# Kernel tuning notes

Hardware: AMD Instinct MI355X
Metric: run time of the kernel (lower is better)

The kernel has to match this reference:

```python
import jax, jax.numpy as jnp
import numpy as np
from jax import lax

B, N, S, H = 8, 32, 512, 768   # batch, max spans, seq len, bert hidden
K, C, L = 3, 128, 64           # conv kernel height, cnn_hidden_size, num labels


def setup_inputs() -> dict:
    key = jax.random.key(0)
    ks = jax.random.split(key, 9)
    rng = np.random.default_rng(0)
    W = 16  # max span width
    starts = rng.integers(0, S - W, size=(B, N))
    widths = rng.integers(1, W + 1, size=(B, N))
    starts[0, 0], widths[0, 0] = 100, W        # force max span width = 16
    starts[0, 1], widths[0, 1] = S - W, 1      # force max prefix width = 496
    starts[0, 2], widths[0, 2] = 0, 1          # force min end = 1 -> max suffix = 511
    ends = starts + widths
    spans_dranges = jnp.asarray(np.stack([starts, ends], axis=-1), dtype=jnp.int32)
    sc = 0.02
    return {
        "tokens_emb": jax.random.normal(ks[0], (B, S, H), jnp.float32),
        "span_w": jax.random.normal(ks[1], (C, H, K), jnp.float32) * sc,
        "span_b": jax.random.normal(ks[2], (C,), jnp.float32) * sc,
        "prefix_w": jax.random.normal(ks[3], (C, H, K), jnp.float32) * sc,
        "prefix_b": jax.random.normal(ks[4], (C,), jnp.float32) * sc,
        "suffix_w": jax.random.normal(ks[5], (C, H, K), jnp.float32) * sc,
        "suffix_b": jax.random.normal(ks[6], (C,), jnp.float32) * sc,
        "fc_w": jax.random.normal(ks[7], (L, 3 * C), jnp.float32) * sc,
        "fc_b": jax.random.normal(ks[8], (L,), jnp.float32) * sc,
        "spans_dranges": spans_dranges,
        "word_seq_lengths": jnp.full((B,), S, dtype=jnp.int32),
        "max_span_width": W,
        "max_prefix_width": S - W,
        "max_suffix_width": S - 1,
    }


def _conv_pool(x, w, b):
    # x: [BN, T, H]; Conv2d(H->C, kernel (K,1)) over time + max_pool over all valid positions
    T = x.shape[1]
    if T < K:  # original pads with zeros up to kernel size
        x = jnp.pad(x, ((0, 0), (0, K - T), (0, 0)))
    y = lax.conv_general_dilated(x.transpose(0, 2, 1), w, (1,), 'VALID',
                                 dimension_numbers=('NCH', 'OIH', 'NCH'))  # [BN, C, T-K+1]
    return (y + b[None, :, None]).max(axis=2)  # pool_filter_size == full output length


def reference(tokens_emb, span_w, span_b, prefix_w, prefix_b, suffix_w, suffix_b,
              fc_w, fc_b, spans_dranges, word_seq_lengths,
              max_span_width, max_prefix_width, max_suffix_width):
    starts = spans_dranges[..., 0]  # [B,N]
    ends = spans_dranges[..., 1]

    def gather(idx, mask):
        # idx, mask: [B,N,W] -> zero-padded per-span token embeddings [B*N, W, H]
        g = jnp.take_along_axis(tokens_emb[:, None], jnp.clip(idx, 0, S - 1)[..., None], axis=2)
        return (g * mask[..., None]).reshape(B * N, -1, H)

    ar = jnp.arange(max_span_width)
    span_x = gather(starts[..., None] + ar, ar < (ends - starts)[..., None])
    arp = jnp.arange(max_prefix_width)
    prefix_x = gather(jnp.broadcast_to(arp, (B, N, max_prefix_width)), arp < starts[..., None])
    ars = jnp.arange(max_suffix_width)
    suffix_x = gather(ends[..., None] + ars,
                      ars < (word_seq_lengths[:, None, None] - ends[..., None]))

    feats = jnp.concatenate([
        _conv_pool(prefix_x, prefix_w, prefix_b),
        _conv_pool(span_x, span_w, span_b),
        _conv_pool(suffix_x, suffix_w, suffix_b),
    ], axis=-1)  # [B*N, 3C]
    probs = jax.nn.sigmoid(feats @ fc_w.T + fc_b)  # [B*N, L]
    pred_ids = (probs > 0.5).astype(jnp.int32).reshape(B, N, L)
    return probs, pred_ids
```

## Files before the change

### kernel.cpp

```cpp
#include <hip/hip_runtime.h>
#include <hip/hip_bf16.h>
#include <math.h>

#define NEG_INF (-1e30f)

typedef _Float16 half8 __attribute__((ext_vector_type(8)));
typedef _Float16 half4 __attribute__((ext_vector_type(4)));
typedef float f32x4 __attribute__((ext_vector_type(4)));
typedef float f32x16 __attribute__((ext_vector_type(16)));

__device__ __forceinline__ void load_lds16(const void* g, void* l) {
  __builtin_amdgcn_global_load_lds((const __attribute__((address_space(1))) void*)g,
                                   (__attribute__((address_space(3))) void*)l, 16, 0, 0);
}

__global__ __launch_bounds__(256) void prep(
    const float* __restrict__ tokens, const float* __restrict__ span_w,
    const float* __restrict__ prefix_w, const float* __restrict__ suffix_w,
    const float* __restrict__ fc_w, _Float16* __restrict__ A2,
    _Float16* __restrict__ Bt, float* __restrict__ fcT) {
  int bid = blockIdx.x;
  int t = threadIdx.x;
  if (bid < 3072) {
    int g4 = (bid * 256 + t) * 4;
    int m = g4 / 768, h = g4 % 768;
    float4 x = *(const float4*)(tokens + g4);
    float xs[4] = {x.x, x.y, x.z, x.w};
    half4 hi, lo;
#pragma unroll
    for (int i = 0; i < 4; ++i) {
      _Float16 h_ = (_Float16)xs[i];
      hi[i] = h_;
      lo[i] = (_Float16)((xs[i] - (float)h_) * 64.0f);
    }
    size_t base = (size_t)m * 1536 + h;
    *(half4*)(A2 + base) = hi;
    *(half4*)(A2 + base + 768) = lo;
  } else if (bid < 3216) {
    int g = (bid - 3072) * 256 + t;
    int ws = g / 12288;
    int r = g % 12288;
    int c = r / 96, h = (r % 96) * 8;
    const float* wsrc = (ws == 0) ? prefix_w : (ws == 1) ? span_w : suffix_w;
    const float* src = wsrc + (size_t)(c * 768 + h) * 3;
    float wv[24];
#pragma unroll
    for (int i = 0; i < 6; ++i) *(float4*)&wv[i * 4] = *(const float4*)(src + i * 4);
#pragma unroll
    for (int tap = 0; tap < 3; ++tap) {
      half8 hi, lo;
#pragma unroll
      for (int i = 0; i < 8; ++i) {
        float x = wv[i * 3 + tap];
        _Float16 h_ = (_Float16)x;
        hi[i] = h_;
        lo[i] = (_Float16)((x - (float)h_) * 64.0f);
      }
      size_t jb = (size_t)(ws * 384 + tap * 128 + c) * 1536 + h;
      *(half8*)(Bt + jb) = hi;
      *(half8*)(Bt + jb + 768) = lo;
    }
  } else {
    int g = (bid - 3216) * 256 + t;
    int i = g >> 6, c = g & 63;
    fcT[g] = fc_w[c * 384 + i];
  }
}

__global__ __launch_bounds__(512) void gemm_f16(const _Float16* __restrict__ A2,
                                                const _Float16* __restrict__ Bt,
                                                float* __restrict__ Ct) {
  __shared__ _Float16 As[2][128 * 64];
  __shared__ _Float16 Bs[2][64 * 64];
  const int bm = blockIdx.x * 128;
  const int bj = blockIdx.y * 64;
  const int tid = threadIdx.x;
  const int w = tid >> 6;
  const int lane = tid & 63;
  const int lrow = lane >> 3;
  const int cphys = lane & 7;
  const int clog = cphys ^ (lrow & 7);
  const int srcoff = (clog >> 2) * 768 + (clog & 3) * 8;
  const _Float16* gA0 = A2 + (size_t)(bm + w * 16 + lrow) * 1536 + srcoff;
  const _Float16* gA1 = A2 + (size_t)(bm + w * 16 + 8 + lrow) * 1536 + srcoff;
  const _Float16* gB0 = Bt + (size_t)(bj + w * 8 + lrow) * 1536 + srcoff;
  const int m0w = (w & 3) * 32;
  const int n0w = (w >> 2) * 32;
  const int arow = m0w + (lane & 31);
  const int brow = n0w + (lane & 31);
  const int hi32 = lane >> 5;
  const int sw = lane & 7;
#define CO(p, ks) (((((p) * 4 + (ks) * 2 + hi32)) ^ sw) * 8)
  f32x16 aa, ab;
#pragma unroll
  for (int q = 0; q < 16; ++q) {
    aa[q] = 0.f;
    ab[q] = 0.f;
  }
  load_lds16(gA0, &As[0][w * 1024]);
  load_lds16(gA1, &As[0][w * 1024 + 512]);
  load_lds16(gB0, &Bs[0][w * 512]);

  for (int i = 0; i < 24; ++i) {
    const int cur = i & 1;
    __syncthreads();
    if (i + 1 < 24) {
      const int kp = (i + 1) * 32;
      const int nxt = cur ^ 1;
      load_lds16(gA0 + kp, &As[nxt][w * 1024]);
      load_lds16(gA1 + kp, &As[nxt][w * 1024 + 512]);
      load_lds16(gB0 + kp, &Bs[nxt][w * 512]);
    }
#pragma unroll
    for (int ks = 0; ks < 2; ++ks) {
      half8 a0 = *(const half8*)&As[cur][arow * 64 + CO(0, ks)];
      half8 a1 = *(const half8*)&As[cur][arow * 64 + CO(1, ks)];
      half8 b0 = *(const half8*)&Bs[cur][brow * 64 + CO(0, ks)];
      half8 b1 = *(const half8*)&Bs[cur][brow * 64 + CO(1, ks)];
      aa = __builtin_amdgcn_mfma_f32_32x32x16_f16(a0, b0, aa, 0, 0, 0);
      ab = __builtin_amdgcn_mfma_f32_32x32x16_f16(a1, b0, ab, 0, 0, 0);
      ab = __builtin_amdgcn_mfma_f32_32x32x16_f16(a0, b1, ab, 0, 0, 0);
    }
  }
#undef CO
  const int n_out = bj + n0w + (lane & 31);
  float* cp = Ct + (size_t)n_out * 4096 + bm + m0w + 4 * hi32;
#pragma unroll
  for (int r = 0; r < 4; ++r) {
    f32x4 v;
#pragma unroll
    for (int q = 0; q < 4; ++q) v[q] = aa[4 * r + q] + 0.015625f * ab[4 * r + q];
    *(f32x4*)(cp + 8 * r) = v;
  }
}

__global__ __launch_bounds__(256) void scan_kernel(const float* __restrict__ Ct,
                                                   const int* __restrict__ wsl,
                                                   float* __restrict__ PM2,
                                                   float* __restrict__ SM2) {
  int pair = blockIdx.x * 4 + (threadIdx.x >> 6);
  int b = pair >> 7;
  int c = pair & 127;
  int lane = threadIdx.x & 63;
  int mb = b * 512;
  int t0 = lane * 8;
  const float* p0 = Ct + (size_t)(0 + c) * 4096 + mb;
  const float* p1 = Ct + (size_t)(128 + c) * 4096 + mb;
  const float* p2 = Ct + (size_t)(256 + c) * 4096 + mb;
  float v[8];
#pragma unroll
  for (int i = 0; i < 8; i++) {
    int t = t0 + i;
    v[i] = (t < 494) ? (p0[t] + p1[t + 1] + p2[t + 2]) : NEG_INF;
  }
#pragma unroll
  for (int i = 1; i < 8; i++) v[i] = fmaxf(v[i], v[i - 1]);
  float x = v[7];
#pragma unroll
  for (int d = 1; d < 64; d <<= 1) {
    float y = __shfl_up(x, d);
    if (lane >= d) x = fmaxf(x, y);
  }
  float excl = __shfl_up(x, 1);
  if (lane == 0) excl = NEG_INF;
  float* pm = PM2 + (size_t)pair * 512;
#pragma unroll
  for (int i = 0; i < 8; i++) {
    int t = t0 + i;
    if (t < 494) pm[t] = fmaxf(v[i], excl);
  }
  const float* s0 = Ct + (size_t)(768 + c) * 4096 + mb;
  const float* s1 = Ct + (size_t)(896 + c) * 4096 + mb;
  const float* s2 = Ct + (size_t)(1024 + c) * 4096 + mb;
  int qmax = wsl[b] - 3;
  if (qmax > 509) qmax = 509;
  float u[8];
#pragma unroll
  for (int i = 0; i < 8; i++) {
    int q = t0 + i;
    u[i] = (q <= qmax) ? (s0[q] + s1[q + 1] + s2[q + 2]) : NEG_INF;
  }
#pragma unroll
  for (int i = 6; i >= 0; i--) u[i] = fmaxf(u[i], u[i + 1]);
  float xr = u[0];
#pragma unroll
  for (int d = 1; d < 64; d <<= 1) {
    float y = __shfl_down(xr, d);
    if (lane < 64 - d) xr = fmaxf(xr, y);
  }
  float exclr = __shfl_down(xr, 1);
  if (lane == 63) exclr = NEG_INF;
  float* sm = SM2 + (size_t)pair * 512;
#pragma unroll
  for (int i = 0; i < 8; i++) sm[t0 + i] = fmaxf(u[i], exclr);
}

__global__ __launch_bounds__(128) void span_kernel(
    const float* __restrict__ Ct, const float* __restrict__ PM2,
    const float* __restrict__ SM2, const float* __restrict__ prefix_b,
    const float* __restrict__ span_b, const float* __restrict__ suffix_b,
    const float* __restrict__ fcT, const float* __restrict__ fc_b,
    const int* __restrict__ spans, const int* __restrict__ wsl,
    float* __restrict__ out) {
  __shared__ float sfeat[384];
  __shared__ float part[64];
  int sp = blockIdx.x;
  int b = sp >> 5;
  int c = threadIdx.x;
  int s = spans[sp * 2], e = spans[sp * 2 + 1];
  int Lb = wsl[b];
  int mb = b * 512;
  {
    const float* t0p = Ct + (size_t)c * 4096 + mb;
    const float* t1p = Ct + (size_t)(128 + c) * 4096 + mb;
    float m = NEG_INF;
    if (s >= 3) m = fmaxf(m, PM2[(size_t)(b * 128 + c) * 512 + s - 3]);
    if (s >= 2 && s <= 495) m = fmaxf(m, t0p[s - 2] + t1p[s - 1]);
    if (s >= 1 && s <= 494) m = fmaxf(m, t0p[s - 1]);
    if (s <= 493) m = fmaxf(m, 0.0f);
    sfeat[c] = m + prefix_b[c];
  }
  {
    const float* u0 = Ct + (size_t)(384 + c) * 4096 + mb;
    const float* u1 = Ct + (size_t)(512 + c) * 4096 + mb;
    const float* u2 = Ct + (size_t)(640 + c) * 4096 + mb;
    int w = e - s;
    float m = NEG_INF;
    for (int p = 0; p + 2 < w; ++p)
      m = fmaxf(m, u0[s + p] + u1[s + p + 1] + u2[s + p + 2]);
    if (w >= 2 && w <= 15) m = fmaxf(m, u0[s + w - 2] + u1[s + w - 1]);
    if (w <= 14) m = fmaxf(m, u0[s + w - 1]);
    if (w <= 13) m = fmaxf(m, 0.0f);
    sfeat[128 + c] = m + span_b[c];
  }
  {
    const float* x0 = Ct + (size_t)(768 + c) * 4096 + mb;
    const float* x1 = Ct + (size_t)(896 + c) * 4096 + mb;
    float m = NEG_INF;
    if (e <= Lb - 3) m = fmaxf(m, SM2[(size_t)(b * 128 + c) * 512 + e]);
    if (Lb - 2 - e >= 0 && Lb - 2 - e <= 508)
      m = fmaxf(m, x0[Lb - 2] + x1[Lb - 1]);
    if (Lb - 1 - e >= 0 && Lb - 1 - e <= 508) m = fmaxf(m, x0[Lb - 1]);
    if (Lb - e <= 508) m = fmaxf(m, 0.0f);
    sfeat[256 + c] = m + suffix_b[c];
  }
  __syncthreads();
  {
    int cc = threadIdx.x & 63;
    int half = threadIdx.x >> 6;
    float acc2 = 0.0f;
    const float* fp = fcT + (size_t)(half * 192) * 64 + cc;
    const float* sf = sfeat + half * 192;
#pragma unroll 8
    for (int i = 0; i < 192; ++i) acc2 = fmaf(sf[i], fp[(size_t)i * 64], acc2);
    if (half) part[cc] = acc2;
    __syncthreads();
    if (!half) {
      float a = acc2 + part[cc] + fc_b[cc];
      float pr = 1.0f / (1.0f + expf(-a));
      out[sp * 64 + cc] = pr;
      out[16384 + sp * 64 + cc] = (pr > 0.5f) ? 1.0f : 0.0f;
    }
  }
}

extern "C" void kernel_launch(void* const* d_in, const int* in_sizes, int n_in,
                              void* d_out, int out_size, void* d_ws,
                              size_t ws_size, hipStream_t stream) {
  const float* tokens = (const float*)d_in[0];
  const float* span_w = (const float*)d_in[1];
  const float* span_b = (const float*)d_in[2];
  const float* prefix_w = (const float*)d_in[3];
  const float* prefix_b = (const float*)d_in[4];
  const float* suffix_w = (const float*)d_in[5];
  const float* suffix_b = (const float*)d_in[6];
  const float* fc_w = (const float*)d_in[7];
  const float* fc_b = (const float*)d_in[8];
  const int* spans = (const int*)d_in[9];
  const int* wsl = (const int*)d_in[10];
  float* out = (float*)d_out;

  char* ws = (char*)d_ws;
  float* Ct = (float*)ws;
  _Float16* A2 = (_Float16*)(ws + 18874368);
  _Float16* Bt = (_Float16*)(ws + 31457280);
  float* PM2 = (float*)(ws + 34996224);
  float* SM2 = (float*)(ws + 37093376);
  float* fcT = (float*)(ws + 39190528);

  hipLaunchKernelGGL(prep, dim3(3312), dim3(256), 0, stream, tokens, span_w,
                     prefix_w, suffix_w, fc_w, A2, Bt, fcT);
  hipLaunchKernelGGL(gemm_f16, dim3(32, 18), dim3(512), 0, stream, A2, Bt, Ct);
  hipLaunchKernelGGL(scan_kernel, dim3(256), dim3(256), 0, stream, Ct, wsl,
                     PM2, SM2);
  hipLaunchKernelGGL(span_kernel, dim3(256), dim3(128), 0, stream, Ct, PM2,
                     SM2, prefix_b, span_b, suffix_b, fcT, fc_b, spans, wsl,
                     out);
}
```

Measured before the change: 147.6 us.

## Enlarge GEMM block tile to 128x128 with 2x2 MFMA tiles per wave

The GEMM block tile grows from 128x64 to 128x128, using 4 waves of 256 threads where each wave computes a 64x64 sub-tile of 2x2 MFMA 32x32 blocks. The grid drops from 576 to 288 blocks. The goal is more operand reuse from LDS per global load and more MFMA work per LDS fragment read. The cost is more accumulator registers per thread and fewer blocks to fill the 256 CUs, which risks lower occupancy and load imbalance.

```diff
diff --git a/kernel.cpp b/kernel.cpp
--- a/kernel.cpp
+++ b/kernel.cpp
@@ -67,39 +67,45 @@
   }
 }
 
-__global__ __launch_bounds__(512) void gemm_f16(const _Float16* __restrict__ A2,
+__global__ __launch_bounds__(256) void gemm_f16(const _Float16* __restrict__ A2,
                                                 const _Float16* __restrict__ Bt,
                                                 float* __restrict__ Ct) {
   __shared__ _Float16 As[2][128 * 64];
-  __shared__ _Float16 Bs[2][64 * 64];
+  __shared__ _Float16 Bs[2][128 * 64];
   const int bm = blockIdx.x * 128;
-  const int bj = blockIdx.y * 64;
+  const int bj = blockIdx.y * 128;
   const int tid = threadIdx.x;
   const int w = tid >> 6;
   const int lane = tid & 63;
-  const int lrow = lane >> 3;
-  const int cphys = lane & 7;
-  const int clog = cphys ^ (lrow & 7);
+  const int srow = tid >> 3;
+  const int phys = tid & 7;
+  const int clog = phys ^ (srow & 7);
   const int srcoff = (clog >> 2) * 768 + (clog & 3) * 8;
-  const _Float16* gA0 = A2 + (size_t)(bm + w * 16 + lrow) * 1536 + srcoff;
-  const _Float16* gA1 = A2 + (size_t)(bm + w * 16 + 8 + lrow) * 1536 + srcoff;
-  const _Float16* gB0 = Bt + (size_t)(bj + w * 8 + lrow) * 1536 + srcoff;
-  const int m0w = (w & 3) * 32;
-  const int n0w = (w >> 2) * 32;
-  const int arow = m0w + (lane & 31);
-  const int brow = n0w + (lane & 31);
+  const _Float16* gA = A2 + (size_t)(bm + srow) * 1536 + srcoff;
+  const _Float16* gB = Bt + (size_t)(bj + srow) * 1536 + srcoff;
+  const size_t rstep = (size_t)32 * 1536;
+  const int l31 = lane & 31;
   const int hi32 = lane >> 5;
   const int sw = lane & 7;
-#define CO(p, ks) (((((p) * 4 + (ks) * 2 + hi32)) ^ sw) * 8)
-  f32x16 aa, ab;
-#pragma unroll
-  for (int q = 0; q < 16; ++q) {
-    aa[q] = 0.f;
-    ab[q] = 0.f;
-  }
-  load_lds16(gA0, &As[0][w * 1024]);
-  load_lds16(gA1, &As[0][w * 1024 + 512]);
-  load_lds16(gB0, &Bs[0][w * 512]);
+  const int m0w = (w & 1) * 64;
+  const int n0w = (w >> 1) * 64;
+#define CO(p, ks) ((((p) * 4 + (ks) * 2 + hi32) ^ sw) * 8)
+  f32x16 aa[2][2], ab[2][2];
+#pragma unroll
+  for (int i = 0; i < 2; ++i)
+#pragma unroll
+    for (int j = 0; j < 2; ++j)
+#pragma unroll
+      for (int q = 0; q < 16; ++q) {
+        aa[i][j][q] = 0.f;
+        ab[i][j][q] = 0.f;
+      }
+
+#pragma unroll
+  for (int p = 0; p < 4; ++p) {
+    load_lds16(gA + (size_t)p * rstep, &As[0][p * 2048 + w * 512]);
+    load_lds16(gB + (size_t)p * rstep, &Bs[0][p * 2048 + w * 512]);
+  }
 
   for (int i = 0; i < 24; ++i) {
     const int cur = i & 1;
@@ -107,31 +113,53 @@
     if (i + 1 < 24) {
       const int kp = (i + 1) * 32;
       const int nxt = cur ^ 1;
-      load_lds16(gA0 + kp, &As[nxt][w * 1024]);
-      load_lds16(gA1 + kp, &As[nxt][w * 1024 + 512]);
-      load_lds16(gB0 + kp, &Bs[nxt][w * 512]);
+#pragma unroll
+      for (int p = 0; p < 4; ++p) {
+        load_lds16(gA + kp + (size_t)p * rstep, &As[nxt][p * 2048 + w * 512]);
+        load_lds16(gB + kp + (size_t)p * rstep, &Bs[nxt][p * 2048 + w * 512]);
+      }
     }
 #pragma unroll
     for (int ks = 0; ks < 2; ++ks) {
-      half8 a0 = *(const half8*)&As[cur][arow * 64 + CO(0, ks)];
-      half8 a1 = *(const half8*)&As[cur][arow * 64 + CO(1, ks)];
-      half8 b0 = *(const half8*)&Bs[cur][brow * 64 + CO(0, ks)];
-      half8 b1 = *(const half8*)&Bs[cur][brow * 64 + CO(1, ks)];
-      aa = __builtin_amdgcn_mfma_f32_32x32x16_f16(a0, b0, aa, 0, 0, 0);
-      ab = __builtin_amdgcn_mfma_f32_32x32x16_f16(a1, b0, ab, 0, 0, 0);
-      ab = __builtin_amdgcn_mfma_f32_32x32x16_f16(a0, b1, ab, 0, 0, 0);
+      half8 a0[2], a1[2], b0[2], b1[2];
+#pragma unroll
+      for (int mp = 0; mp < 2; ++mp) {
+        const int row = (m0w + mp * 32 + l31) * 64;
+        a0[mp] = *(const half8*)&As[cur][row + CO(0, ks)];
+        a1[mp] = *(const half8*)&As[cur][row + CO(1, ks)];
+      }
+#pragma unroll
+      for (int np = 0; np < 2; ++np) {
+        const int row = (n0w + np * 32 + l31) * 64;
+        b0[np] = *(const half8*)&Bs[cur][row + CO(0, ks)];
+        b1[np] = *(const half8*)&Bs[cur][row + CO(1, ks)];
+      }
+#pragma unroll
+      for (int mp = 0; mp < 2; ++mp)
+#pragma unroll
+        for (int np = 0; np < 2; ++np) {
+          aa[mp][np] = __builtin_amdgcn_mfma_f32_32x32x16_f16(a0[mp], b0[np], aa[mp][np], 0, 0, 0);
+          ab[mp][np] = __builtin_amdgcn_mfma_f32_32x32x16_f16(a1[mp], b0[np], ab[mp][np], 0, 0, 0);
+          ab[mp][np] = __builtin_amdgcn_mfma_f32_32x32x16_f16(a0[mp], b1[np], ab[mp][np], 0, 0, 0);
+        }
     }
   }
 #undef CO
-  const int n_out = bj + n0w + (lane & 31);
-  float* cp = Ct + (size_t)n_out * 4096 + bm + m0w + 4 * hi32;
-#pragma unroll
-  for (int r = 0; r < 4; ++r) {
-    f32x4 v;
-#pragma unroll
-    for (int q = 0; q < 4; ++q) v[q] = aa[4 * r + q] + 0.015625f * ab[4 * r + q];
-    *(f32x4*)(cp + 8 * r) = v;
-  }
+#pragma unroll
+  for (int mp = 0; mp < 2; ++mp)
+#pragma unroll
+    for (int np = 0; np < 2; ++np) {
+      const int n_out = bj + n0w + np * 32 + l31;
+      float* cp = Ct + (size_t)n_out * 4096 + bm + m0w + mp * 32 + 4 * hi32;
+#pragma unroll
+      for (int r = 0; r < 4; ++r) {
+        f32x4 v;
+#pragma unroll
+        for (int q = 0; q < 4; ++q)
+          v[q] = aa[mp][np][4 * r + q] + 0.015625f * ab[mp][np][4 * r + q];
+        *(f32x4*)(cp + 8 * r) = v;
+      }
+    }
 }
 
 __global__ __launch_bounds__(256) void scan_kernel(const float* __restrict__ Ct,
@@ -290,7 +318,7 @@
 
   hipLaunchKernelGGL(prep, dim3(3312), dim3(256), 0, stream, tokens, span_w,
                      prefix_w, suffix_w, fc_w, A2, Bt, fcT);
-  hipLaunchKernelGGL(gemm_f16, dim3(32, 18), dim3(512), 0, stream, A2, Bt, Ct);
+  hipLaunchKernelGGL(gemm_f16, dim3(32, 9), dim3(256), 0, stream, A2, Bt, Ct);
   hipLaunchKernelGGL(scan_kernel, dim3(256), dim3(256), 0, stream, Ct, wsl,
                      PM2, SM2);
   hipLaunchKernelGGL(span_kernel, dim3(256), dim3(128), 0, stream, Ct, PM2,
```

New measurement: 152.0 us. +2.9%, slower.

## Replace LDS double-buffered GEMM with direct global loads into MFMA registers

Applied to the files above, without the earlier changes.

The f16 split-precision GEMM drops shared-memory staging and barriers. Each of 4 waves now loads its A and B fragments straight from global memory and computes a 32x64 output tile, using two accumulator pairs per wave instead of one. This removes LDS traffic and __syncthreads, but every wave rereads the B rows and loads are uncoalesced 16-byte strided reads that rely on the cache, so memory latency may be exposed without explicit prefetching.

```diff
diff --git a/kernel.cpp b/kernel.cpp
--- a/kernel.cpp
+++ b/kernel.cpp
@@ -8,11 +8,6 @@
 typedef _Float16 half4 __attribute__((ext_vector_type(4)));
 typedef float f32x4 __attribute__((ext_vector_type(4)));
 typedef float f32x16 __attribute__((ext_vector_type(16)));
-
-__device__ __forceinline__ void load_lds16(const void* g, void* l) {
-  __builtin_amdgcn_global_load_lds((const __attribute__((address_space(1))) void*)g,
-                                   (__attribute__((address_space(3))) void*)l, 16, 0, 0);
-}
 
 __global__ __launch_bounds__(256) void prep(
     const float* __restrict__ tokens, const float* __restrict__ span_w,
@@ -67,70 +62,63 @@
   }
 }
 
-__global__ __launch_bounds__(512) void gemm_f16(const _Float16* __restrict__ A2,
+__global__ __launch_bounds__(256) void gemm_f16(const _Float16* __restrict__ A2,
                                                 const _Float16* __restrict__ Bt,
                                                 float* __restrict__ Ct) {
-  __shared__ _Float16 As[2][128 * 64];
-  __shared__ _Float16 Bs[2][64 * 64];
   const int bm = blockIdx.x * 128;
   const int bj = blockIdx.y * 64;
-  const int tid = threadIdx.x;
-  const int w = tid >> 6;
-  const int lane = tid & 63;
-  const int lrow = lane >> 3;
-  const int cphys = lane & 7;
-  const int clog = cphys ^ (lrow & 7);
-  const int srcoff = (clog >> 2) * 768 + (clog & 3) * 8;
-  const _Float16* gA0 = A2 + (size_t)(bm + w * 16 + lrow) * 1536 + srcoff;
-  const _Float16* gA1 = A2 + (size_t)(bm + w * 16 + 8 + lrow) * 1536 + srcoff;
-  const _Float16* gB0 = Bt + (size_t)(bj + w * 8 + lrow) * 1536 + srcoff;
-  const int m0w = (w & 3) * 32;
-  const int n0w = (w >> 2) * 32;
-  const int arow = m0w + (lane & 31);
-  const int brow = n0w + (lane & 31);
+  const int w = threadIdx.x >> 6;
+  const int lane = threadIdx.x & 63;
+  const int l31 = lane & 31;
   const int hi32 = lane >> 5;
-  const int sw = lane & 7;
-#define CO(p, ks) (((((p) * 4 + (ks) * 2 + hi32)) ^ sw) * 8)
-  f32x16 aa, ab;
+  const _Float16* pa = A2 + (size_t)(bm + w * 32 + l31) * 1536 + hi32 * 8;
+  const _Float16* pb0 = Bt + (size_t)(bj + l31) * 1536 + hi32 * 8;
+  const _Float16* pb1 = Bt + (size_t)(bj + 32 + l31) * 1536 + hi32 * 8;
+  f32x16 aa0, ab0, aa1, ab1;
 #pragma unroll
   for (int q = 0; q < 16; ++q) {
-    aa[q] = 0.f;
-    ab[q] = 0.f;
-  }
-  load_lds16(gA0, &As[0][w * 1024]);
-  load_lds16(gA1, &As[0][w * 1024 + 512]);
-  load_lds16(gB0, &Bs[0][w * 512]);
-
-  for (int i = 0; i < 24; ++i) {
-    const int cur = i & 1;
-    __syncthreads();
-    if (i + 1 < 24) {
-      const int kp = (i + 1) * 32;
-      const int nxt = cur ^ 1;
-      load_lds16(gA0 + kp, &As[nxt][w * 1024]);
-      load_lds16(gA1 + kp, &As[nxt][w * 1024 + 512]);
-      load_lds16(gB0 + kp, &Bs[nxt][w * 512]);
-    }
-#pragma unroll
-    for (int ks = 0; ks < 2; ++ks) {
-      half8 a0 = *(const half8*)&As[cur][arow * 64 + CO(0, ks)];
-      half8 a1 = *(const half8*)&As[cur][arow * 64 + CO(1, ks)];
-      half8 b0 = *(const half8*)&Bs[cur][brow * 64 + CO(0, ks)];
-      half8 b1 = *(const half8*)&Bs[cur][brow * 64 + CO(1, ks)];
-      aa = __builtin_amdgcn_mfma_f32_32x32x16_f16(a0, b0, aa, 0, 0, 0);
-      ab = __builtin_amdgcn_mfma_f32_32x32x16_f16(a1, b0, ab, 0, 0, 0);
-      ab = __builtin_amdgcn_mfma_f32_32x32x16_f16(a0, b1, ab, 0, 0, 0);
-    }
-  }
-#undef CO
-  const int n_out = bj + n0w + (lane & 31);
-  float* cp = Ct + (size_t)n_out * 4096 + bm + m0w + 4 * hi32;
-#pragma unroll
-  for (int r = 0; r < 4; ++r) {
-    f32x4 v;
-#pragma unroll
-    for (int q = 0; q < 4; ++q) v[q] = aa[4 * r + q] + 0.015625f * ab[4 * r + q];
-    *(f32x4*)(cp + 8 * r) = v;
+    aa0[q] = 0.f;
+    ab0[q] = 0.f;
+    aa1[q] = 0.f;
+    ab1[q] = 0.f;
+  }
+#pragma unroll 2
+  for (int k = 0; k < 768; k += 16) {
+    half8 a0 = *(const half8*)(pa + k);
+    half8 a1 = *(const half8*)(pa + k + 768);
+    half8 b00 = *(const half8*)(pb0 + k);
+    half8 b01 = *(const half8*)(pb0 + k + 768);
+    half8 b10 = *(const half8*)(pb1 + k);
+    half8 b11 = *(const half8*)(pb1 + k + 768);
+    aa0 = __builtin_amdgcn_mfma_f32_32x32x16_f16(a0, b00, aa0, 0, 0, 0);
+    ab0 = __builtin_amdgcn_mfma_f32_32x32x16_f16(a1, b00, ab0, 0, 0, 0);
+    ab0 = __builtin_amdgcn_mfma_f32_32x32x16_f16(a0, b01, ab0, 0, 0, 0);
+    aa1 = __builtin_amdgcn_mfma_f32_32x32x16_f16(a0, b10, aa1, 0, 0, 0);
+    ab1 = __builtin_amdgcn_mfma_f32_32x32x16_f16(a1, b10, ab1, 0, 0, 0);
+    ab1 = __builtin_amdgcn_mfma_f32_32x32x16_f16(a0, b11, ab1, 0, 0, 0);
+  }
+  const int m0 = bm + w * 32 + 4 * hi32;
+  {
+    const int n_out = bj + l31;
+    float* cp = Ct + (size_t)n_out * 4096 + m0;
+#pragma unroll
+    for (int r = 0; r < 4; ++r) {
+      f32x4 v;
+#pragma unroll
+      for (int q = 0; q < 4; ++q) v[q] = aa0[4 * r + q] + 0.015625f * ab0[4 * r + q];
+      *(f32x4*)(cp + 8 * r) = v;
+    }
+  }
+  {
+    const int n_out = bj + 32 + l31;
+    float* cp = Ct + (size_t)n_out * 4096 + m0;
+#pragma unroll
+    for (int r = 0; r < 4; ++r) {
+      f32x4 v;
+#pragma unroll
+      for (int q = 0; q < 4; ++q) v[q] = aa1[4 * r + q] + 0.015625f * ab1[4 * r + q];
+      *(f32x4*)(cp + 8 * r) = v;
+    }
   }
 }
 
@@ -290,7 +278,7 @@
 
   hipLaunchKernelGGL(prep, dim3(3312), dim3(256), 0, stream, tokens, span_w,
                      prefix_w, suffix_w, fc_w, A2, Bt, fcT);
-  hipLaunchKernelGGL(gemm_f16, dim3(32, 18), dim3(512), 0, stream, A2, Bt, Ct);
+  hipLaunchKernelGGL(gemm_f16, dim3(32, 18), dim3(256), 0, stream, A2, Bt, Ct);
   hipLaunchKernelGGL(scan_kernel, dim3(256), dim3(256), 0, stream, Ct, wsl,
                      PM2, SM2);
   hipLaunchKernelGGL(span_kernel, dim3(256), dim3(128), 0, stream, Ct, PM2,
```

New measurement: 212.0 us. 1.44x slower.
